# Kernel optimization log

Hardware: AMD Instinct MI355X
Metric: run time of the kernel (lower is better)

## Reference

```python
import jax, jax.numpy as jnp
import numpy as np

B, T, E = 4, 2048, 1024
NH = 16            # num_heads
DH = E // NH       # per-head dim
NE = 2048          # num_experts = block_size (literal constructor wiring)
HID = NH           # expert hidden_dim = num_heads (literal constructor wiring)
EPS = 1e-5


def setup_inputs() -> dict:
    key = jax.random.key(0)
    ks = jax.random.split(key, 12)
    s = 0.02
    return {
        "x": jax.random.normal(ks[0], (B, T, E), jnp.float32),
        "ln1_g": jnp.ones((E,), jnp.float32),
        "ln1_b": jnp.zeros((E,), jnp.float32),
        "ln2_g": jnp.ones((E,), jnp.float32),
        "ln2_b": jnp.zeros((E,), jnp.float32),
        "qkv_w": jax.random.normal(ks[1], (E, 3 * E), jnp.float32) * s,
        "qkv_b": jnp.zeros((3 * E,), jnp.float32),
        "proj_w": jax.random.normal(ks[2], (E, E), jnp.float32) * s,
        "proj_b": jnp.zeros((E,), jnp.float32),
        "gate_w": jax.random.normal(ks[3], (E, NE), jnp.float32) * s,
        "gate_b": jnp.zeros((NE,), jnp.float32),
        "w1": jax.random.normal(ks[4], (NE, E, HID), jnp.float32) * s,
        "b1": jnp.zeros((NE, HID), jnp.float32),
        "w2": jax.random.normal(ks[5], (NE, HID, E), jnp.float32) * s,
        "b2": jnp.zeros((NE, E), jnp.float32),
    }


def _layernorm(x, g, b):
    mu = jnp.mean(x, axis=-1, keepdims=True)
    var = jnp.mean(jnp.square(x - mu), axis=-1, keepdims=True)
    return (x - mu) * jax.lax.rsqrt(var + EPS) * g + b


def _attention(h, qkv_w, qkv_b, proj_w, proj_b):
    qkv = h @ qkv_w + qkv_b                       # [B,T,3E]
    qkv = qkv.reshape(h.shape[0], h.shape[1], 3, NH, DH)
    q, k, v = qkv[:, :, 0], qkv[:, :, 1], qkv[:, :, 2]   # [B,T,NH,DH]
    scores = jnp.einsum('bqhd,bkhd->bhqk', q, k) * (DH ** -0.5)
    causal = jnp.tril(jnp.ones((h.shape[1], h.shape[1]), bool))
    scores = jnp.where(causal, scores, -jnp.inf)
    attn = jax.nn.softmax(scores, axis=-1)
    out = jnp.einsum('bhqk,bkhd->bqhd', attn, v).reshape(h.shape[0], h.shape[1], E)
    return out @ proj_w + proj_b


def _moe(h, gate_w, gate_b, w1, b1, w2, b2):
    # top-1 routing via argmax of gate softmax (== argmax of logits)
    logits = h @ gate_w + gate_b                  # [B,T,NE]
    idx = jnp.argmax(logits, axis=-1)             # [B,T]
    xf = h.reshape(-1, E)                         # [N,E]
    fidx = idx.reshape(-1)                        # [N]
    tw1 = w1[fidx]                                # [N,E,HID]
    tb1 = b1[fidx]                                # [N,HID]
    tw2 = w2[fidx]                                # [N,HID,E]
    tb2 = b2[fidx]                                # [N,E]
    hmid = jax.nn.gelu(jnp.einsum('ne,neh->nh', xf, tw1) + tb1, approximate=False)
    yf = jnp.einsum('nh,nhe->ne', hmid, tw2) + tb2
    return yf.reshape(h.shape)


def reference(x, ln1_g, ln1_b, ln2_g, ln2_b, qkv_w, qkv_b, proj_w, proj_b,
              gate_w, gate_b, w1, b1, w2, b2):
    x = x + _attention(_layernorm(x, ln1_g, ln1_b), qkv_w, qkv_b, proj_w, proj_b)
    x = x + _moe(_layernorm(x, ln2_g, ln2_b), gate_w, gate_b, w1, b1, w2, b2)
    return x
```

## Files before the change

kernel.cpp:

```cpp
#include <hip/hip_runtime.h>
#include <math.h>

#define TOKENS 8192
#define EDIM   1024
#define TSEQ   2048
#define NEXP   2048

typedef __attribute__((ext_vector_type(8))) short short8;
typedef __attribute__((ext_vector_type(4))) float f32x4;

__device__ __forceinline__ short f2bf(float f) {
  union { float f; unsigned u; } c; c.f = f;
  unsigned r = c.u + 0x7fffu + ((c.u >> 16) & 1u);
  return (short)(r >> 16);
}
__device__ __forceinline__ float bf2f(short h) {
  union { unsigned u; float f; } c; c.u = ((unsigned)(unsigned short)h) << 16;
  return c.f;
}
__device__ __forceinline__ void split3(float a, short& p0, short& p1, short& p2) {
  p0 = f2bf(a);
  float r = a - bf2f(p0);
  p1 = f2bf(r);
  p2 = f2bf(r - bf2f(p1));
}

__global__ __launch_bounds__(256) void ln_kernel(const float* __restrict__ x,
    const float* __restrict__ g, const float* __restrict__ b,
    short* __restrict__ obf, float* __restrict__ of32)
{
  const int row = blockIdx.x;
  const int t = threadIdx.x, lane = t & 63, w = t >> 6;
  const float4 v = ((const float4*)(x + (size_t)row * EDIM))[t];
  __shared__ float lds[4];
  float s = v.x + v.y + v.z + v.w;
  #pragma unroll
  for (int m = 32; m >= 1; m >>= 1) s += __shfl_xor(s, m);
  if (lane == 0) lds[w] = s;
  __syncthreads();
  const float mu = (lds[0] + lds[1] + lds[2] + lds[3]) * (1.f / EDIM);
  __syncthreads();
  const float d0 = v.x - mu, d1 = v.y - mu, d2 = v.z - mu, d3 = v.w - mu;
  float sq = d0 * d0 + d1 * d1 + d2 * d2 + d3 * d3;
  #pragma unroll
  for (int m = 32; m >= 1; m >>= 1) sq += __shfl_xor(sq, m);
  if (lane == 0) lds[w] = sq;
  __syncthreads();
  const float var = (lds[0] + lds[1] + lds[2] + lds[3]) * (1.f / EDIM);
  const float rstd = rsqrtf(var + 1e-5f);
  const float4 gg = ((const float4*)g)[t];
  const float4 bb = ((const float4*)b)[t];
  const float y0 = d0 * rstd * gg.x + bb.x;
  const float y1 = d1 * rstd * gg.y + bb.y;
  const float y2 = d2 * rstd * gg.z + bb.z;
  const float y3 = d3 * rstd * gg.w + bb.w;
  if (obf) {
    unsigned long long pk =
        (unsigned long long)(unsigned short)f2bf(y0)
      | ((unsigned long long)(unsigned short)f2bf(y1) << 16)
      | ((unsigned long long)(unsigned short)f2bf(y2) << 32)
      | ((unsigned long long)(unsigned short)f2bf(y3) << 48);
    *(unsigned long long*)(obf + (size_t)row * EDIM + t * 4) = pk;
  }
  ((float4*)(of32 + (size_t)row * EDIM))[t] = make_float4(y0, y1, y2, y3);
}

__global__ __launch_bounds__(256) void wsplit_kernel(const float* __restrict__ W,
    short* __restrict__ Wt, int K, int N)
{
  __shared__ float tile[32][33];
  const int n0 = blockIdx.x * 32, k0 = blockIdx.y * 32;
  const int tx = threadIdx.x & 31, ty = threadIdx.x >> 5;
  #pragma unroll
  for (int i = 0; i < 4; i++)
    tile[ty * 4 + i][tx] = W[(size_t)(k0 + ty * 4 + i) * N + n0 + tx];
  __syncthreads();
  const size_t PS = (size_t)N * K;
  #pragma unroll
  for (int i = 0; i < 4; i++) {
    short p0, p1, p2;
    split3(tile[tx][ty * 4 + i], p0, p1, p2);
    const size_t idx = (size_t)(n0 + ty * 4 + i) * K + k0 + tx;
    Wt[idx] = p0; Wt[PS + idx] = p1; Wt[2 * PS + idx] = p2;
  }
}

__global__ __launch_bounds__(256) void wconv_kernel(const float* __restrict__ W,
    short* __restrict__ Wt, int K, int N)
{
  __shared__ float tile[32][33];
  const int n0 = blockIdx.x * 32, k0 = blockIdx.y * 32;
  const int tx = threadIdx.x & 31, ty = threadIdx.x >> 5;
  #pragma unroll
  for (int i = 0; i < 4; i++)
    tile[ty * 4 + i][tx] = W[(size_t)(k0 + ty * 4 + i) * N + n0 + tx];
  __syncthreads();
  #pragma unroll
  for (int i = 0; i < 4; i++)
    Wt[(size_t)(n0 + ty * 4 + i) * K + k0 + tx] = f2bf(tile[tx][ty * 4 + i]);
}

template<int ADD_RES>
__global__ __launch_bounds__(256) void gemm_hp(const float* __restrict__ A,
    const short* __restrict__ Bp, size_t bstride, const float* __restrict__ bias,
    const float* __restrict__ resid, float* __restrict__ outp,
    int M, int N, int K)
{
  __shared__ short As[3][128][40];
  __shared__ short Bs[3][128][40];
  const int m0 = blockIdx.y * 128, n0 = blockIdx.x * 128;
  const int t = threadIdx.x;
  const int lane = t & 63, w = t >> 6;
  const int wm = w >> 1, wn = w & 1;
  const int lo = lane & 15, hi = lane >> 4;
  const int srow = t >> 1, sc0 = (t & 1) * 16;
  f32x4 acc[4][4];
  #pragma unroll
  for (int i = 0; i < 4; i++)
    #pragma unroll
    for (int j = 0; j < 4; j++)
      acc[i][j] = (f32x4){0.f, 0.f, 0.f, 0.f};

  for (int k0 = 0; k0 < K; k0 += 32) {
    {
      const float* ap = A + (size_t)(m0 + srow) * K + k0 + sc0;
      float av[16];
      *(float4*)&av[0]  = *(const float4*)ap;
      *(float4*)&av[4]  = *(const float4*)(ap + 4);
      *(float4*)&av[8]  = *(const float4*)(ap + 8);
      *(float4*)&av[12] = *(const float4*)(ap + 12);
      short pl[3][16];
      #pragma unroll
      for (int e = 0; e < 16; e++) split3(av[e], pl[0][e], pl[1][e], pl[2][e]);
      #pragma unroll
      for (int p = 0; p < 3; p++) {
        *(short8*)&As[p][srow][sc0]     = *(short8*)&pl[p][0];
        *(short8*)&As[p][srow][sc0 + 8] = *(short8*)&pl[p][8];
      }
    }
    #pragma unroll
    for (int p = 0; p < 3; p++) {
      const short* bp = Bp + (size_t)p * bstride + (size_t)(n0 + srow) * K + k0 + sc0;
      *(uint4*)&Bs[p][srow][sc0]     = *(const uint4*)bp;
      *(uint4*)&Bs[p][srow][sc0 + 8] = *(const uint4*)(bp + 8);
    }
    __syncthreads();
    short8 af[3][4], bf[3][4];
    #pragma unroll
    for (int p = 0; p < 3; p++)
      #pragma unroll
      for (int i = 0; i < 4; i++) {
        af[p][i] = *(const short8*)(&As[p][wm * 64 + i * 16 + lo][hi * 8]);
        bf[p][i] = *(const short8*)(&Bs[p][wn * 64 + i * 16 + lo][hi * 8]);
      }
    #pragma unroll
    for (int i = 0; i < 4; i++)
      #pragma unroll
      for (int j = 0; j < 4; j++) {
        acc[i][j] = __builtin_amdgcn_mfma_f32_16x16x32_bf16(af[0][i], bf[0][j], acc[i][j], 0, 0, 0);
        acc[i][j] = __builtin_amdgcn_mfma_f32_16x16x32_bf16(af[0][i], bf[1][j], acc[i][j], 0, 0, 0);
        acc[i][j] = __builtin_amdgcn_mfma_f32_16x16x32_bf16(af[1][i], bf[0][j], acc[i][j], 0, 0, 0);
        acc[i][j] = __builtin_amdgcn_mfma_f32_16x16x32_bf16(af[1][i], bf[1][j], acc[i][j], 0, 0, 0);
        acc[i][j] = __builtin_amdgcn_mfma_f32_16x16x32_bf16(af[0][i], bf[2][j], acc[i][j], 0, 0, 0);
        acc[i][j] = __builtin_amdgcn_mfma_f32_16x16x32_bf16(af[2][i], bf[0][j], acc[i][j], 0, 0, 0);
      }
    __syncthreads();
  }
  #pragma unroll
  for (int i = 0; i < 4; i++)
    #pragma unroll
    for (int j = 0; j < 4; j++)
      #pragma unroll
      for (int r = 0; r < 4; r++) {
        const int gm = m0 + wm * 64 + i * 16 + hi * 4 + r;
        const int gn = n0 + wn * 64 + j * 16 + lo;
        float v = acc[i][j][r] + bias[gn];
        if (ADD_RES) v += resid[(size_t)gm * N + gn];
        outp[(size_t)gm * N + gn] = v;
      }
}

__global__ __launch_bounds__(256) void attn_hp(const float* __restrict__ qkvf,
    float* __restrict__ attno)
{
  const int bh = blockIdx.x;
  const int b = bh >> 4, h = bh & 15;
  const int qb0 = blockIdx.y * 64;
  const int t = threadIdx.x, lane = t & 63, w = t >> 6;
  const int lo = lane & 15, hi = lane >> 4;
  __shared__ short Ks[3][32][72];
  __shared__ short Vs[3][64][40];
  __shared__ short Ps[3][4][16][40];
  const size_t base = (size_t)b * TSEQ * 3072;
  const int qw0 = qb0 + w * 16;
  short8 qf[3][2];
  #pragma unroll
  for (int c = 0; c < 2; c++) {
    const float* qp = qkvf + base + (size_t)(qw0 + lo) * 3072 + h * 64 + c * 32 + hi * 8;
    float qv[8];
    *(float4*)&qv[0] = *(const float4*)qp;
    *(float4*)&qv[4] = *(const float4*)(qp + 4);
    #pragma unroll
    for (int j = 0; j < 8; j++) {
      short s0, s1, s2;
      split3(qv[j], s0, s1, s2);
      qf[0][c][j] = s0; qf[1][c][j] = s1; qf[2][c][j] = s2;
    }
  }
  float m_r[4], l_r[4];
  f32x4 o[4];
  #pragma unroll
  for (int r = 0; r < 4; r++) { m_r[r] = -INFINITY; l_r[r] = 0.f; }
  #pragma unroll
  for (int nb = 0; nb < 4; nb++) o[nb] = (f32x4){0.f, 0.f, 0.f, 0.f};

  const int ntiles = 2 * blockIdx.y + 2;
  for (int tile = 0; tile < ntiles; tile++) {
    const int kt0 = tile * 32;
    {
      const int key = t >> 3, c0 = (t & 7) * 8;
      const float* kp = qkvf + base + (size_t)(kt0 + key) * 3072 + 1024 + h * 64 + c0;
      float kv[8];
      *(float4*)&kv[0] = *(const float4*)kp;
      *(float4*)&kv[4] = *(const float4*)(kp + 4);
      short kpl[3][8];
      #pragma unroll
      for (int j = 0; j < 8; j++) split3(kv[j], kpl[0][j], kpl[1][j], kpl[2][j]);
      #pragma unroll
      for (int p = 0; p < 3; p++) *(short8*)&Ks[p][key][c0] = *(short8*)&kpl[p][0];
      float vv[8];
      *(float4*)&vv[0] = *(const float4*)(kp + 1024);
      *(float4*)&vv[4] = *(const float4*)(kp + 1028);
      #pragma unroll
      for (int j = 0; j < 8; j++) {
        short v0, v1, v2;
        split3(vv[j], v0, v1, v2);
        Vs[0][c0 + j][key] = v0; Vs[1][c0 + j][key] = v1; Vs[2][c0 + j][key] = v2;
      }
    }
    __syncthreads();
    if (kt0 <= qw0 + 15) {
      f32x4 s[2];
      #pragma unroll
      for (int kb = 0; kb < 2; kb++) {
        f32x4 z = (f32x4){0.f, 0.f, 0.f, 0.f};
        #pragma unroll
        for (int c = 0; c < 2; c++) {
          const short8 kf0 = *(const short8*)(&Ks[0][kb * 16 + lo][c * 32 + hi * 8]);
          const short8 kf1 = *(const short8*)(&Ks[1][kb * 16 + lo][c * 32 + hi * 8]);
          const short8 kf2 = *(const short8*)(&Ks[2][kb * 16 + lo][c * 32 + hi * 8]);
          z = __builtin_amdgcn_mfma_f32_16x16x32_bf16(qf[0][c], kf0, z, 0, 0, 0);
          z = __builtin_amdgcn_mfma_f32_16x16x32_bf16(qf[0][c], kf1, z, 0, 0, 0);
          z = __builtin_amdgcn_mfma_f32_16x16x32_bf16(qf[1][c], kf0, z, 0, 0, 0);
          z = __builtin_amdgcn_mfma_f32_16x16x32_bf16(qf[1][c], kf1, z, 0, 0, 0);
          z = __builtin_amdgcn_mfma_f32_16x16x32_bf16(qf[0][c], kf2, z, 0, 0, 0);
          z = __builtin_amdgcn_mfma_f32_16x16x32_bf16(qf[2][c], kf0, z, 0, 0, 0);
        }
        s[kb] = z;
      }
      float alpha[4];
      #pragma unroll
      for (int r = 0; r < 4; r++) {
        const int qg = qw0 + hi * 4 + r;
        float tm = -1e30f;
        #pragma unroll
        for (int kb = 0; kb < 2; kb++) {
          float v = s[kb][r] * 0.125f;
          const int kg = kt0 + kb * 16 + lo;
          v = (kg > qg) ? -1e30f : v;
          s[kb][r] = v;
          tm = fmaxf(tm, v);
        }
        #pragma unroll
        for (int mm = 8; mm >= 1; mm >>= 1) tm = fmaxf(tm, __shfl_xor(tm, mm));
        const float mn = fmaxf(m_r[r], tm);
        alpha[r] = __expf(m_r[r] - mn);
        float ps = 0.f;
        #pragma unroll
        for (int kb = 0; kb < 2; kb++) {
          const float pv = __expf(s[kb][r] - mn);
          s[kb][r] = pv;
          ps += pv;
        }
        #pragma unroll
        for (int mm = 8; mm >= 1; mm >>= 1) ps += __shfl_xor(ps, mm);
        l_r[r] = l_r[r] * alpha[r] + ps;
        m_r[r] = mn;
      }
      #pragma unroll
      for (int nb = 0; nb < 4; nb++) {
        o[nb][0] *= alpha[0]; o[nb][1] *= alpha[1];
        o[nb][2] *= alpha[2]; o[nb][3] *= alpha[3];
      }
      #pragma unroll
      for (int kb = 0; kb < 2; kb++)
        #pragma unroll
        for (int r = 0; r < 4; r++) {
          short p0, p1, p2;
          split3(s[kb][r], p0, p1, p2);
          Ps[0][w][hi * 4 + r][kb * 16 + lo] = p0;
          Ps[1][w][hi * 4 + r][kb * 16 + lo] = p1;
          Ps[2][w][hi * 4 + r][kb * 16 + lo] = p2;
        }
      __threadfence_block();
      const short8 pf0 = *(const short8*)(&Ps[0][w][lo][hi * 8]);
      const short8 pf1 = *(const short8*)(&Ps[1][w][lo][hi * 8]);
      const short8 pf2 = *(const short8*)(&Ps[2][w][lo][hi * 8]);
      #pragma unroll
      for (int nb = 0; nb < 4; nb++) {
        const short8 vb0 = *(const short8*)(&Vs[0][nb * 16 + lo][hi * 8]);
        const short8 vb1 = *(const short8*)(&Vs[1][nb * 16 + lo][hi * 8]);
        const short8 vb2 = *(const short8*)(&Vs[2][nb * 16 + lo][hi * 8]);
        o[nb] = __builtin_amdgcn_mfma_f32_16x16x32_bf16(pf0, vb0, o[nb], 0, 0, 0);
        o[nb] = __builtin_amdgcn_mfma_f32_16x16x32_bf16(pf0, vb1, o[nb], 0, 0, 0);
        o[nb] = __builtin_amdgcn_mfma_f32_16x16x32_bf16(pf1, vb0, o[nb], 0, 0, 0);
        o[nb] = __builtin_amdgcn_mfma_f32_16x16x32_bf16(pf1, vb1, o[nb], 0, 0, 0);
        o[nb] = __builtin_amdgcn_mfma_f32_16x16x32_bf16(pf0, vb2, o[nb], 0, 0, 0);
        o[nb] = __builtin_amdgcn_mfma_f32_16x16x32_bf16(pf2, vb0, o[nb], 0, 0, 0);
      }
    }
    __syncthreads();
  }
  #pragma unroll
  for (int nb = 0; nb < 4; nb++)
    #pragma unroll
    for (int r = 0; r < 4; r++) {
      const int tok = qw0 + hi * 4 + r;
      attno[(size_t)(b * TSEQ + tok) * EDIM + h * 64 + nb * 16 + lo] = o[nb][r] / l_r[r];
    }
}

__global__ __launch_bounds__(256) void gemm_bf16(const short* __restrict__ A,
    const short* __restrict__ Bt, const float* __restrict__ bias,
    float* __restrict__ outp, int M, int N, int K)
{
  __shared__ short As[128][72];
  __shared__ short Bs[128][72];
  const int m0 = blockIdx.y * 128, n0 = blockIdx.x * 128;
  const int t = threadIdx.x;
  const int lane = t & 63, w = t >> 6;
  const int wm = w >> 1, wn = w & 1;
  const int lo = lane & 15, hi = lane >> 4;
  f32x4 acc[4][4];
  #pragma unroll
  for (int i = 0; i < 4; i++)
    #pragma unroll
    for (int j = 0; j < 4; j++)
      acc[i][j] = (f32x4){0.f, 0.f, 0.f, 0.f};
  for (int k0 = 0; k0 < K; k0 += 64) {
    #pragma unroll
    for (int c = 0; c < 4; c++) {
      const int cc = t + 256 * c;
      const int row = cc >> 3, col = (cc & 7) * 8;
      *(uint4*)(&As[row][col]) = *(const uint4*)(A + (size_t)(m0 + row) * K + k0 + col);
      *(uint4*)(&Bs[row][col]) = *(const uint4*)(Bt + (size_t)(n0 + row) * K + k0 + col);
    }
    __syncthreads();
    #pragma unroll
    for (int kk = 0; kk < 2; kk++) {
      short8 af[4], bf[4];
      #pragma unroll
      for (int i = 0; i < 4; i++) {
        af[i] = *(const short8*)(&As[wm * 64 + i * 16 + lo][kk * 32 + hi * 8]);
        bf[i] = *(const short8*)(&Bs[wn * 64 + i * 16 + lo][kk * 32 + hi * 8]);
      }
      #pragma unroll
      for (int i = 0; i < 4; i++)
        #pragma unroll
        for (int j = 0; j < 4; j++)
          acc[i][j] = __builtin_amdgcn_mfma_f32_16x16x32_bf16(af[i], bf[j], acc[i][j], 0, 0, 0);
    }
    __syncthreads();
  }
  #pragma unroll
  for (int i = 0; i < 4; i++)
    #pragma unroll
    for (int j = 0; j < 4; j++)
      #pragma unroll
      for (int r = 0; r < 4; r++) {
        const int gm = m0 + wm * 64 + i * 16 + hi * 4 + r;
        const int gn = n0 + wn * 64 + j * 16 + lo;
        outp[(size_t)gm * N + gn] = acc[i][j][r] + bias[gn];
      }
}

__global__ __launch_bounds__(256) void gate_argmax(const float* __restrict__ logits,
    const float* __restrict__ h2f, const float* __restrict__ gw,
    const float* __restrict__ gb, int* __restrict__ eidx)
{
  const int token = blockIdx.x;
  const int t = threadIdx.x, lane = t & 63, w = t >> 6;
  const float* row = logits + (size_t)token * NEXP;
  float bm = -1e30f;
  #pragma unroll
  for (int c = 0; c < 8; c++) bm = fmaxf(bm, row[t + 256 * c]);
  #pragma unroll
  for (int m = 32; m >= 1; m >>= 1) bm = fmaxf(bm, __shfl_xor(bm, m));
  __shared__ float wred[4];
  __shared__ int cnt;
  __shared__ int cand[16];
  __shared__ float sred[4];
  if (t == 0) cnt = 0;
  if (lane == 0) wred[w] = bm;
  __syncthreads();
  const float maxv = fmaxf(fmaxf(wred[0], wred[1]), fmaxf(wred[2], wred[3]));
  const float thr = maxv - 0.03f;
  #pragma unroll
  for (int c = 0; c < 8; c++) {
    const int e = t + 256 * c;
    if (row[e] > thr) {
      const int p = atomicAdd(&cnt, 1);
      if (p < 16) cand[p] = e;
    }
  }
  __syncthreads();
  const int nc = cnt < 16 ? cnt : 16;
  if (nc == 1) {
    if (t == 0) eidx[token] = cand[0];
    return;
  }
  const float* xr = h2f + (size_t)token * EDIM;
  int best = NEXP; float bs = -1e30f;
  for (int c = 0; c < nc; c++) {
    const int e = cand[c];
    float p = 0.f;
    #pragma unroll
    for (int ii = 0; ii < 4; ii++) {
      const int i = t + 256 * ii;
      p += xr[i] * gw[(size_t)i * NEXP + e];
    }
    #pragma unroll
    for (int m = 32; m >= 1; m >>= 1) p += __shfl_xor(p, m);
    if (lane == 0) sred[w] = p;
    __syncthreads();
    const float s = sred[0] + sred[1] + sred[2] + sred[3] + gb[e];
    if (s > bs || (s == bs && e < best)) { bs = s; best = e; }
    __syncthreads();
  }
  if (t == 0) eidx[token] = best;
}

__global__ __launch_bounds__(256) void moe_kernel(const float* __restrict__ h2f,
    const int* __restrict__ eidx, const float* __restrict__ w1,
    const float* __restrict__ b1, const float* __restrict__ w2,
    const float* __restrict__ b2, float* __restrict__ out)
{
  const int token = blockIdx.x;
  const int t = threadIdx.x, lane = t & 63, w = t >> 6;
  const int e = eidx[token];
  const float* xr = h2f + (size_t)token * EDIM;
  const float* w1e = w1 + (size_t)e * (EDIM * 16);
  float acc[16];
  #pragma unroll
  for (int hh = 0; hh < 16; hh++) acc[hh] = 0.f;
  #pragma unroll
  for (int ii = 0; ii < 4; ii++) {
    const int i = t + 256 * ii;
    const float xi = xr[i];
    const float4* wr = (const float4*)(w1e + (size_t)i * 16);
    const float4 r0 = wr[0], r1 = wr[1], r2 = wr[2], r3 = wr[3];
    acc[0] = fmaf(xi, r0.x, acc[0]);  acc[1] = fmaf(xi, r0.y, acc[1]);
    acc[2] = fmaf(xi, r0.z, acc[2]);  acc[3] = fmaf(xi, r0.w, acc[3]);
    acc[4] = fmaf(xi, r1.x, acc[4]);  acc[5] = fmaf(xi, r1.y, acc[5]);
    acc[6] = fmaf(xi, r1.z, acc[6]);  acc[7] = fmaf(xi, r1.w, acc[7]);
    acc[8] = fmaf(xi, r2.x, acc[8]);  acc[9] = fmaf(xi, r2.y, acc[9]);
    acc[10] = fmaf(xi, r2.z, acc[10]); acc[11] = fmaf(xi, r2.w, acc[11]);
    acc[12] = fmaf(xi, r3.x, acc[12]); acc[13] = fmaf(xi, r3.y, acc[13]);
    acc[14] = fmaf(xi, r3.z, acc[14]); acc[15] = fmaf(xi, r3.w, acc[15]);
  }
  #pragma unroll
  for (int hh = 0; hh < 16; hh++)
    #pragma unroll
    for (int m = 32; m >= 1; m >>= 1) acc[hh] += __shfl_xor(acc[hh], m);
  __shared__ float red[4][16];
  __shared__ float hm[16];
  if (lane == 0) {
    #pragma unroll
    for (int hh = 0; hh < 16; hh++) red[w][hh] = acc[hh];
  }
  __syncthreads();
  if (t < 16) {
    const float s = red[0][t] + red[1][t] + red[2][t] + red[3][t] + b1[(size_t)e * 16 + t];
    hm[t] = 0.5f * s * (1.f + erff(s * 0.70710678118654752f));
  }
  __syncthreads();
  const float* w2e = w2 + (size_t)e * (16 * EDIM);
  float4 y = *(const float4*)(b2 + (size_t)e * EDIM + t * 4);
  const float4 res = *(const float4*)(out + (size_t)token * EDIM + t * 4);
  y.x += res.x; y.y += res.y; y.z += res.z; y.w += res.w;
  #pragma unroll
  for (int hh = 0; hh < 16; hh++) {
    const float hv = hm[hh];
    const float4 wv = *(const float4*)(w2e + (size_t)hh * EDIM + t * 4);
    y.x = fmaf(hv, wv.x, y.x);
    y.y = fmaf(hv, wv.y, y.y);
    y.z = fmaf(hv, wv.z, y.z);
    y.w = fmaf(hv, wv.w, y.w);
  }
  *(float4*)(out + (size_t)token * EDIM + t * 4) = y;
}

extern "C" void kernel_launch(void* const* d_in, const int* in_sizes, int n_in,
                              void* d_out, int out_size, void* d_ws, size_t ws_size,
                              hipStream_t stream) {
  const float* x      = (const float*)d_in[0];
  const float* ln1_g  = (const float*)d_in[1];
  const float* ln1_b  = (const float*)d_in[2];
  const float* ln2_g  = (const float*)d_in[3];
  const float* ln2_b  = (const float*)d_in[4];
  const float* qkv_w  = (const float*)d_in[5];
  const float* qkv_b  = (const float*)d_in[6];
  const float* proj_w = (const float*)d_in[7];
  const float* proj_b = (const float*)d_in[8];
  const float* gate_w = (const float*)d_in[9];
  const float* gate_b = (const float*)d_in[10];
  const float* w1     = (const float*)d_in[11];
  const float* b1     = (const float*)d_in[12];
  const float* w2     = (const float*)d_in[13];
  const float* b2     = (const float*)d_in[14];
  float* out = (float*)d_out;

  char* p = (char*)d_ws;
  short* wTq = (short*)p; p += 3ull * 3072 * 1024 * 2;
  short* wTp = (short*)p; p += 3ull * 1024 * 1024 * 2;
  short* wTg = (short*)p; p += 2048ull * 1024 * 2;
  short* h2  = (short*)p; p += (size_t)TOKENS * EDIM * 2;
  int* eidx  = (int*)p;   p += (size_t)TOKENS * 4;
  p = (char*)(((size_t)p + 255) & ~(size_t)255);
  float* R1  = (float*)p; p += (size_t)TOKENS * EDIM * 4;
  float* R2  = (float*)p; p += (size_t)TOKENS * 3072 * 4;
  float* h1f = R1;
  float* attnof = R1;
  float* h2f = R1;
  float* qkvf = R2;
  float* logits = R2;

  wsplit_kernel<<<dim3(3072 / 32, 1024 / 32), 256, 0, stream>>>(qkv_w, wTq, 1024, 3072);
  wsplit_kernel<<<dim3(1024 / 32, 1024 / 32), 256, 0, stream>>>(proj_w, wTp, 1024, 1024);
  wconv_kernel<<<dim3(2048 / 32, 1024 / 32), 256, 0, stream>>>(gate_w, wTg, 1024, 2048);

  ln_kernel<<<TOKENS, 256, 0, stream>>>(x, ln1_g, ln1_b, nullptr, h1f);
  gemm_hp<0><<<dim3(3072 / 128, TOKENS / 128), 256, 0, stream>>>(
      h1f, wTq, (size_t)3072 * 1024, qkv_b, nullptr, qkvf, TOKENS, 3072, 1024);
  attn_hp<<<dim3(64, TSEQ / 64), 256, 0, stream>>>(qkvf, attnof);
  gemm_hp<1><<<dim3(1024 / 128, TOKENS / 128), 256, 0, stream>>>(
      attnof, wTp, (size_t)1024 * 1024, proj_b, x, out, TOKENS, 1024, 1024);
  ln_kernel<<<TOKENS, 256, 0, stream>>>(out, ln2_g, ln2_b, h2, h2f);
  gemm_bf16<<<dim3(2048 / 128, TOKENS / 128), 256, 0, stream>>>(
      h2, wTg, gate_b, logits, TOKENS, 2048, 1024);
  gate_argmax<<<TOKENS, 256, 0, stream>>>(logits, h2f, gate_w, gate_b, eidx);
  moe_kernel<<<TOKENS, 256, 0, stream>>>(h2f, eidx, w1, b1, w2, b2, out);
}
```

Before: 1.426 ms.

## Precompute bf16-split K and transposed V planes before attention

Adds two pre-pass kernels that split K into three bf16 planes and transpose and split V into per-head d-major bf16 planes in global memory. The attention kernel then loads these planes directly into shared memory with vector loads, instead of redoing the fp32 split and scattered transposed LDS stores for every query block. This removes redundant split work, which was repeated across query tiles, and the strided LDS writes. The cost is two extra launches, extra global traffic and workspace, and smaller LDS padding (stride 32) that may cause bank conflicts.

```diff
diff --git a/kernel.cpp b/kernel.cpp
--- a/kernel.cpp
+++ b/kernel.cpp
@@ -100,6 +100,50 @@
     Wt[(size_t)(n0 + ty * 4 + i) * K + k0 + tx] = f2bf(tile[tx][ty * 4 + i]);
 }
 
+__global__ __launch_bounds__(256) void ksplit_kernel(const float* __restrict__ qkvf,
+    short* __restrict__ Kp)
+{
+  const size_t gid = (size_t)blockIdx.x * 256 + threadIdx.x;
+  const int tok = (int)(gid >> 7);
+  const int c = (int)(gid & 127) * 8;
+  const float* src = qkvf + (size_t)tok * 3072 + 1024 + c;
+  float v[8];
+  *(float4*)&v[0] = *(const float4*)src;
+  *(float4*)&v[4] = *(const float4*)(src + 4);
+  short pl[3][8];
+  #pragma unroll
+  for (int j = 0; j < 8; j++) split3(v[j], pl[0][j], pl[1][j], pl[2][j]);
+  const size_t PS = (size_t)TOKENS * EDIM;
+  const size_t dst = (size_t)tok * EDIM + c;
+  *(short8*)(Kp + dst)          = *(short8*)&pl[0][0];
+  *(short8*)(Kp + PS + dst)     = *(short8*)&pl[1][0];
+  *(short8*)(Kp + 2 * PS + dst) = *(short8*)&pl[2][0];
+}
+
+__global__ __launch_bounds__(256) void vtrans_kernel(const float* __restrict__ qkvf,
+    short* __restrict__ Vt)
+{
+  __shared__ float tile[32][33];
+  const int bh = blockIdx.x;
+  const int b = bh >> 4, h = bh & 15;
+  const int t0 = blockIdx.y * 32;
+  const int d0 = blockIdx.z * 32;
+  const int tx = threadIdx.x & 31, ty = threadIdx.x >> 5;
+  #pragma unroll
+  for (int i = 0; i < 4; i++)
+    tile[ty * 4 + i][tx] =
+        qkvf[(size_t)(b * TSEQ + t0 + ty * 4 + i) * 3072 + 2048 + h * 64 + d0 + tx];
+  __syncthreads();
+  const size_t PS = (size_t)64 * 64 * TSEQ;
+  #pragma unroll
+  for (int i = 0; i < 4; i++) {
+    short p0, p1, p2;
+    split3(tile[tx][ty * 4 + i], p0, p1, p2);
+    const size_t idx = (size_t)(bh * 64 + d0 + ty * 4 + i) * TSEQ + t0 + tx;
+    Vt[idx] = p0; Vt[PS + idx] = p1; Vt[2 * PS + idx] = p2;
+  }
+}
+
 template<int ADD_RES>
 __global__ __launch_bounds__(256) void gemm_hp(const float* __restrict__ A,
     const short* __restrict__ Bp, size_t bstride, const float* __restrict__ bias,
@@ -181,6 +225,7 @@
 }
 
 __global__ __launch_bounds__(256) void attn_hp(const float* __restrict__ qkvf,
+    const short* __restrict__ Kp, const short* __restrict__ Vt,
     float* __restrict__ attno)
 {
   const int bh = blockIdx.x;
@@ -189,9 +234,11 @@
   const int t = threadIdx.x, lane = t & 63, w = t >> 6;
   const int lo = lane & 15, hi = lane >> 4;
   __shared__ short Ks[3][32][72];
-  __shared__ short Vs[3][64][40];
-  __shared__ short Ps[3][4][16][40];
+  __shared__ short Vs[3][64][32];
+  __shared__ short Ps[3][4][16][32];
   const size_t base = (size_t)b * TSEQ * 3072;
+  const size_t PSK = (size_t)TOKENS * EDIM;
+  const size_t PSV = (size_t)64 * 64 * TSEQ;
   const int qw0 = qb0 + w * 16;
   short8 qf[3][2];
   #pragma unroll
@@ -219,24 +266,15 @@
     const int kt0 = tile * 32;
     {
       const int key = t >> 3, c0 = (t & 7) * 8;
-      const float* kp = qkvf + base + (size_t)(kt0 + key) * 3072 + 1024 + h * 64 + c0;
-      float kv[8];
-      *(float4*)&kv[0] = *(const float4*)kp;
-      *(float4*)&kv[4] = *(const float4*)(kp + 4);
-      short kpl[3][8];
-      #pragma unroll
-      for (int j = 0; j < 8; j++) split3(kv[j], kpl[0][j], kpl[1][j], kpl[2][j]);
-      #pragma unroll
-      for (int p = 0; p < 3; p++) *(short8*)&Ks[p][key][c0] = *(short8*)&kpl[p][0];
-      float vv[8];
-      *(float4*)&vv[0] = *(const float4*)(kp + 1024);
-      *(float4*)&vv[4] = *(const float4*)(kp + 1028);
-      #pragma unroll
-      for (int j = 0; j < 8; j++) {
-        short v0, v1, v2;
-        split3(vv[j], v0, v1, v2);
-        Vs[0][c0 + j][key] = v0; Vs[1][c0 + j][key] = v1; Vs[2][c0 + j][key] = v2;
-      }
+      const short* kp = Kp + (size_t)(b * TSEQ + kt0 + key) * EDIM + h * 64 + c0;
+      *(short8*)&Ks[0][key][c0] = *(const short8*)kp;
+      *(short8*)&Ks[1][key][c0] = *(const short8*)(kp + PSK);
+      *(short8*)&Ks[2][key][c0] = *(const short8*)(kp + 2 * PSK);
+      const int d = t >> 2, kc = (t & 3) * 8;
+      const short* vp = Vt + (size_t)(bh * 64 + d) * TSEQ + kt0 + kc;
+      *(short8*)&Vs[0][d][kc] = *(const short8*)vp;
+      *(short8*)&Vs[1][d][kc] = *(const short8*)(vp + PSV);
+      *(short8*)&Vs[2][d][kc] = *(const short8*)(vp + 2 * PSV);
     }
     __syncthreads();
     if (kt0 <= qw0 + 15) {
@@ -529,6 +567,8 @@
   p = (char*)(((size_t)p + 255) & ~(size_t)255);
   float* R1  = (float*)p; p += (size_t)TOKENS * EDIM * 4;
   float* R2  = (float*)p; p += (size_t)TOKENS * 3072 * 4;
+  short* Kp  = (short*)p; p += 3ull * TOKENS * EDIM * 2;
+  short* Vt  = (short*)p; p += 3ull * 64 * 64 * TSEQ * 2;
   float* h1f = R1;
   float* attnof = R1;
   float* h2f = R1;
@@ -542,7 +582,9 @@
   ln_kernel<<<TOKENS, 256, 0, stream>>>(x, ln1_g, ln1_b, nullptr, h1f);
   gemm_hp<0><<<dim3(3072 / 128, TOKENS / 128), 256, 0, stream>>>(
       h1f, wTq, (size_t)3072 * 1024, qkv_b, nullptr, qkvf, TOKENS, 3072, 1024);
-  attn_hp<<<dim3(64, TSEQ / 64), 256, 0, stream>>>(qkvf, attnof);
+  ksplit_kernel<<<TOKENS * 128 / 256, 256, 0, stream>>>(qkvf, Kp);
+  vtrans_kernel<<<dim3(64, TSEQ / 32, 2), 256, 0, stream>>>(qkvf, Vt);
+  attn_hp<<<dim3(64, TSEQ / 64), 256, 0, stream>>>(qkvf, Kp, Vt, attnof);
   gemm_hp<1><<<dim3(1024 / 128, TOKENS / 128), 256, 0, stream>>>(
       attnof, wTp, (size_t)1024 * 1024, proj_b, x, out, TOKENS, 1024, 1024);
   ln_kernel<<<TOKENS, 256, 0, stream>>>(out, ln2_g, ln2_b, h2, h2f);
```

Measured after the change: 1.307 ms. 1.09x faster.
